# Kernel optimization log

Measured on AMD Instinct MI355X. Metric: run time of the kernel, lower is better.

The kernel has to match this reference:

```python
import jax, jax.numpy as jnp
import numpy as np

D = 128
N1, N2, N3, N4 = 100000, 200000, 300000, 400000


def setup_inputs() -> dict:
    key = jax.random.key(0)
    cnt = [0]

    def nrm(shape, scale=0.05):
        cnt[0] += 1
        return jax.random.normal(jax.random.fold_in(key, cnt[0]), shape, dtype=jnp.float32) * scale

    def rint(shape, hi):
        cnt[0] += 1
        return jax.random.randint(jax.random.fold_in(key, cnt[0]), shape, 0, hi)

    inp = {}
    inp["h"] = nrm((N1, D), 1.0)
    inp["idx2"] = rint((N2, 2), N1)
    inp["idx3"] = rint((N3, 3), N1)
    inp["idx4"] = rint((N4, 4), N1)
    # sequential_%L MLPs: Linear(L*D -> D) + relu, Linear(D->D)+relu, Linear(D->D)+relu
    for L in (1, 2, 3, 4):
        din = D * L
        inp["s%d_W0" % L] = nrm((din, D))
        inp["s%d_b0" % L] = nrm((D,))
        inp["s%d_W1" % L] = nrm((D, D))
        inp["s%d_b1" % L] = nrm((D,))
        inp["s%d_W2" % L] = nrm((D, D))
        inp["s%d_b2" % L] = nrm((D,))
    # per-feature output heads Linear(D -> 1)
    for f in ("sigma", "epsilon", "q"):
        inp["h1_%s_W" % f] = nrm((D, 1))
        inp["h1_%s_b" % f] = nrm((1,))
    for L in (2, 3, 4):
        for f in ("k", "eq"):
            inp["h%d_%s_W" % (L, f)] = nrm((D, 1))
            inp["h%d_%s_b" % (L, f)] = nrm((1,))
    return inp


def _mlp(x, W0, b0, W1, b1, W2, b2):
    x = jax.nn.relu(x @ W0 + b0)
    x = jax.nn.relu(x @ W1 + b1)
    return jax.nn.relu(x @ W2 + b2)


def _level(h, idx, p):
    # copy_u + mean with exactly one n1 neighbor per relationship slot == gather
    g = jnp.take(h, idx, axis=0)              # [N, K, D]
    N, K, Dd = g.shape
    xf = g.reshape(N, K * Dd)                 # concat h0..h_{K-1}
    xb = g[:, ::-1, :].reshape(N, K * Dd)     # concat reversed
    return _mlp(xf, *p) + _mlp(xb, *p)        # pool = torch.add


def reference(h, idx2, idx3, idx4,
              s1_W0, s1_b0, s1_W1, s1_b1, s1_W2, s1_b2,
              s2_W0, s2_b0, s2_W1, s2_b1, s2_W2, s2_b2,
              s3_W0, s3_b0, s3_W1, s3_b1, s3_W2, s3_b2,
              s4_W0, s4_b0, s4_W1, s4_b1, s4_W2, s4_b2,
              h1_sigma_W, h1_sigma_b, h1_epsilon_W, h1_epsilon_b, h1_q_W, h1_q_b,
              h2_k_W, h2_k_b, h2_eq_W, h2_eq_b,
              h3_k_W, h3_k_b, h3_eq_W, h3_eq_b,
              h4_k_W, h4_k_b, h4_eq_W, h4_eq_b):
    y1 = _mlp(h, s1_W0, s1_b0, s1_W1, s1_b1, s1_W2, s1_b2)
    sigma = y1 @ h1_sigma_W + h1_sigma_b
    epsilon = y1 @ h1_epsilon_W + h1_epsilon_b
    q = y1 @ h1_q_W + h1_q_b
    y2 = _level(h, idx2, (s2_W0, s2_b0, s2_W1, s2_b1, s2_W2, s2_b2))
    k2 = y2 @ h2_k_W + h2_k_b
    eq2 = y2 @ h2_eq_W + h2_eq_b
    y3 = _level(h, idx3, (s3_W0, s3_b0, s3_W1, s3_b1, s3_W2, s3_b2))
    k3 = y3 @ h3_k_W + h3_k_b
    eq3 = y3 @ h3_eq_W + h3_eq_b
    y4 = _level(h, idx4, (s4_W0, s4_b0, s4_W1, s4_b1, s4_W2, s4_b2))
    k4 = y4 @ h4_k_W + h4_k_b
    eq4 = y4 @ h4_eq_W + h4_eq_b
    return (sigma, epsilon, q, k2, eq2, k3, eq3, k4, eq4)
```

## Files before the change

### kernel.cpp

```cpp
#include <hip/hip_runtime.h>

typedef __attribute__((ext_vector_type(8))) _Float16 half8;
typedef __attribute__((ext_vector_type(4))) float f32x4;

#define N1_ 100000
#define N2_ 200000
#define N3_ 300000
#define N4_ 400000

typedef __attribute__((address_space(1))) const void gconst_t;
typedef __attribute__((address_space(3))) void lds_t;

__device__ __forceinline__ unsigned short f2h_bits(float x) {
  union { _Float16 h; unsigned short u; } cv;
  cv.h = (_Float16)x;
  return cv.u;
}

__device__ __forceinline__ f32x4 mfma16(half8 a, half8 b, f32x4 c) {
  return __builtin_amdgcn_mfma_f32_16x16x32_f16(a, b, c, 0, 0, 0);
}

__global__ void cvt_h_kernel(const float* __restrict__ h,
                             unsigned short* __restrict__ hf, int n4) {
  int i = blockIdx.x * blockDim.x + threadIdx.x;
  if (i >= n4) return;
  float4 v = reinterpret_cast<const float4*>(h)[i];
  ushort4 o;
  o.x = f2h_bits(v.x); o.y = f2h_bits(v.y);
  o.z = f2h_bits(v.z); o.w = f2h_bits(v.w);
  reinterpret_cast<ushort4*>(hf)[i] = o;
}

struct PackInfo {
  const float* W[12];
  int kt_base[13];
  int out_off[12];
};

__global__ void pack_w_kernel(PackInfo info, unsigned short* __restrict__ pw) {
  int b = blockIdx.x;
  int lane = threadIdx.x;
  int m = 0;
  while (m < 11 && b >= info.kt_base[m + 1]) ++m;
  int kt = b - info.kt_base[m];
  const float* W = info.W[m];
  int lr = lane & 15, kb = lane >> 4;
  unsigned short* outp = pw + info.out_off[m] + (size_t)kt * 4096 + lane * 8;
  #pragma unroll
  for (int nt = 0; nt < 8; ++nt) {
    #pragma unroll
    for (int j = 0; j < 8; ++j) {
      int krow = kt * 32 + kb * 8 + j;
      int col = nt * 16 + lr;
      outp[nt * 512 + j] = f2h_bits(W[(size_t)krow * 128 + col]);
    }
  }
}

template <int K, int NHEAD>
__global__ __launch_bounds__(256, 2) void level_kernel(
    const unsigned short* __restrict__ hf,
    const int* __restrict__ idx,
    const unsigned short* __restrict__ pw,
    const float* __restrict__ b0, const float* __restrict__ b1,
    const float* __restrict__ b2,
    const float* __restrict__ hw0, const float* __restrict__ hb0,
    float* __restrict__ out0,
    const float* __restrict__ hw1, const float* __restrict__ hb1,
    float* __restrict__ out1,
    const float* __restrict__ hw2, const float* __restrict__ hb2,
    float* __restrict__ out2,
    int N) {
  constexpr int NDIR = (K > 1) ? 2 : 1;
  constexpr int KT0 = 4 * K;
  constexpr int NPAIR = (K / 2) * 4;
  constexpr bool MID = (K % 2) != 0;

  __shared__ __align__(16) unsigned short bstage[2][4096];
  __shared__ __align__(16) unsigned short act[4][NDIR][2][2048];

  const int lane = threadIdx.x & 63;
  const int wid = threadIdx.x >> 6;
  const int lrow = lane & 15;
  const int kb = lane >> 4;

  const int wtile = (blockIdx.x * 4 + wid) * 2;
  const int maxtile = N / 16 - 1;
  int tile[2];
  bool wr[2];
  #pragma unroll
  for (int t = 0; t < 2; ++t) {
    wr[t] = (wtile + t <= maxtile);
    tile[t] = wr[t] ? (wtile + t) : maxtile;
  }

  int src[2][K];
  #pragma unroll
  for (int t = 0; t < 2; ++t)
    #pragma unroll
    for (int s = 0; s < K; ++s)
      src[t][s] = (K == 1) ? (tile[t] * 16 + lrow)
                           : idx[(size_t)(tile[t] * 16 + lrow) * K + s];

  auto stage = [&](int buf, const unsigned short* slab) {
    const unsigned short* g = slab + (wid * 2) * 512 + lane * 8;
    unsigned short* l = &bstage[buf][(wid * 2) * 512];
    __builtin_amdgcn_global_load_lds((gconst_t*)g, (lds_t*)l, 16, 0, 0);
    __builtin_amdgcn_global_load_lds((gconst_t*)(g + 512), (lds_t*)(l + 512), 16, 0, 0);
  };

  auto gfrag = [&](int segRow, int sub, half8* dst) {
    #pragma unroll
    for (int t = 0; t < 2; ++t)
      dst[t] = *reinterpret_cast<const half8*>(
          hf + (size_t)src[t][segRow] * 128 + sub * 32 + kb * 8);
  };

  f32x4 acc[2][NDIR][8];
  auto zero_acc = [&]() {
    #pragma unroll
    for (int t = 0; t < 2; ++t)
      #pragma unroll
      for (int d = 0; d < NDIR; ++d)
        #pragma unroll
        for (int nt = 0; nt < 8; ++nt) acc[t][d][nt] = f32x4{0.f, 0.f, 0.f, 0.f};
  };

  auto mfma_phase = [&](int buf, half8* af, half8* ab) {
    #pragma unroll
    for (int nt = 0; nt < 8; ++nt) {
      half8 bq = *reinterpret_cast<const half8*>(&bstage[buf][nt * 512 + lane * 8]);
      #pragma unroll
      for (int t = 0; t < 2; ++t) {
        acc[t][0][nt] = mfma16(af[t], bq, acc[t][0][nt]);
        if constexpr (NDIR == 2) acc[t][1][nt] = mfma16(ab[t], bq, acc[t][1][nt]);
      }
    }
  };

  auto actA = [&](int t, int d, int kt) -> half8 {
    unsigned off = (unsigned)(lrow * 256 + (kt * 32 + kb * 8) * 2) ^
                   ((unsigned)(lrow & 7) << 4);
    return *reinterpret_cast<const half8*>(
        reinterpret_cast<const unsigned char*>(&act[wid][d][t][0]) + off);
  };

  auto store_act = [&](int t, int d, const float* bias) {
    unsigned char* base = reinterpret_cast<unsigned char*>(&act[wid][d][t][0]);
    #pragma unroll
    for (int nt = 0; nt < 8; ++nt) {
      float bv = bias[nt * 16 + lrow];
      #pragma unroll
      for (int r = 0; r < 4; ++r) {
        float v = fmaxf(acc[t][d][nt][r] + bv, 0.f);
        int trow = 4 * kb + r;
        unsigned off = (unsigned)(trow * 256 + (nt * 16 + lrow) * 2) ^
                       ((unsigned)(trow & 7) << 4);
        *reinterpret_cast<unsigned short*>(base + off) = f2h_bits(v);
      }
    }
  };

  int cur = 0;
  zero_acc();

  half8 gA[2], gB[2], nA[2], nB[2];
  stage(cur, pw);
  gfrag(0, 0, gA);
  if constexpr (NPAIR > 0) gfrag(K - 1, 0, gB);
  __syncthreads();

  for (int pr = 0; pr < NPAIR; ++pr) {
    const int sp = pr >> 2, sub = pr & 3;
    const int slabB = (K - 1 - sp) * 4 + sub;
    stage(cur ^ 1, pw + (size_t)slabB * 4096);
    mfma_phase(cur, gA, gB);
    __syncthreads();
    cur ^= 1;
    if (pr + 1 < NPAIR) {
      const int sp2 = (pr + 1) >> 2, sub2 = (pr + 1) & 3;
      stage(cur ^ 1, pw + (size_t)(sp2 * 4 + sub2) * 4096);
      gfrag(sp2, sub2, nA);
      gfrag(K - 1 - sp2, sub2, nB);
    } else if constexpr (MID) {
      stage(cur ^ 1, pw + (size_t)(((K - 1) / 2) * 4) * 4096);
      gfrag((K - 1) / 2, 0, nA);
    } else {
      stage(cur ^ 1, pw + (size_t)KT0 * 4096);
    }
    mfma_phase(cur, gB, gA);
    __syncthreads();
    cur ^= 1;
    #pragma unroll
    for (int t = 0; t < 2; ++t) { gA[t] = nA[t]; gB[t] = nB[t]; }
  }

  if constexpr (MID) {
    const int mseg = (K - 1) / 2;
    for (int sub = 0; sub < 4; ++sub) {
      if (sub + 1 < 4) {
        stage(cur ^ 1, pw + (size_t)(mseg * 4 + sub + 1) * 4096);
        gfrag(mseg, sub + 1, nA);
      } else {
        stage(cur ^ 1, pw + (size_t)KT0 * 4096);
      }
      mfma_phase(cur, gA, gA);
      __syncthreads();
      cur ^= 1;
      #pragma unroll
      for (int t = 0; t < 2; ++t) gA[t] = nA[t];
    }
  }

  #pragma unroll
  for (int t = 0; t < 2; ++t)
    #pragma unroll
    for (int d = 0; d < NDIR; ++d) store_act(t, d, b0);

  const unsigned short* w1 = pw + (size_t)KT0 * 4096;
  #pragma unroll 1
  for (int layer = 1; layer <= 2; ++layer) {
    const unsigned short* w = (layer == 1) ? w1 : w1 + 16384;
    zero_acc();
    for (int kt = 0; kt < 4; ++kt) {
      if (kt + 1 < 4) stage(cur ^ 1, w + (size_t)(kt + 1) * 4096);
      else if (layer == 1) stage(cur ^ 1, w1 + 16384);
      half8 a[2][NDIR];
      #pragma unroll
      for (int t = 0; t < 2; ++t)
        #pragma unroll
        for (int d = 0; d < NDIR; ++d) a[t][d] = actA(t, d, kt);
      #pragma unroll
      for (int nt = 0; nt < 8; ++nt) {
        half8 bq = *reinterpret_cast<const half8*>(&bstage[cur][nt * 512 + lane * 8]);
        #pragma unroll
        for (int t = 0; t < 2; ++t)
          #pragma unroll
          for (int d = 0; d < NDIR; ++d)
            acc[t][d][nt] = mfma16(a[t][d], bq, acc[t][d][nt]);
      }
      if (!(layer == 2 && kt == 3)) {
        __syncthreads();
        cur ^= 1;
      }
    }
    if (layer == 1) {
      #pragma unroll
      for (int t = 0; t < 2; ++t)
        #pragma unroll
        for (int d = 0; d < NDIR; ++d) store_act(t, d, b1);
    }
  }

  const float* hws[3] = {hw0, hw1, hw2};
  const float* hbs[3] = {hb0, hb1, hb2};
  float* outs[3] = {out0, out1, out2};

  #pragma unroll
  for (int t = 0; t < 2; ++t) {
    f32x4 y[8];
    #pragma unroll
    for (int nt = 0; nt < 8; ++nt) {
      float bv = b2[nt * 16 + lrow];
      #pragma unroll
      for (int r = 0; r < 4; ++r) {
        float v = fmaxf(acc[t][0][nt][r] + bv, 0.f);
        if constexpr (NDIR == 2) v += fmaxf(acc[t][1][nt][r] + bv, 0.f);
        y[nt][r] = v;
      }
    }
    #pragma unroll
    for (int hd = 0; hd < NHEAD; ++hd) {
      float p[4] = {0.f, 0.f, 0.f, 0.f};
      #pragma unroll
      for (int nt = 0; nt < 8; ++nt) {
        float w = hws[hd][nt * 16 + lrow];
        #pragma unroll
        for (int r = 0; r < 4; ++r) p[r] += y[nt][r] * w;
      }
      #pragma unroll
      for (int m = 1; m < 16; m <<= 1) {
        #pragma unroll
        for (int r = 0; r < 4; ++r) p[r] += __shfl_xor(p[r], m, 64);
      }
      if (wr[t] && lrow < 4) {
        float pv = (lrow == 0) ? p[0] : (lrow == 1) ? p[1] : (lrow == 2) ? p[2] : p[3];
        outs[hd][tile[t] * 16 + 4 * kb + lrow] = pv + hbs[hd][0];
      }
    }
  }
}

extern "C" void kernel_launch(void* const* d_in, const int* in_sizes, int n_in,
                              void* d_out, int out_size, void* d_ws, size_t ws_size,
                              hipStream_t stream) {
  (void)in_sizes; (void)n_in; (void)out_size;

  const float* h = (const float*)d_in[0];
  const int* idx2 = (const int*)d_in[1];
  const int* idx3 = (const int*)d_in[2];
  const int* idx4 = (const int*)d_in[3];

  const float* sW[4][3];
  const float* sb[4][3];
  for (int L = 0; L < 4; ++L)
    for (int j = 0; j < 3; ++j) {
      sW[L][j] = (const float*)d_in[4 + L * 6 + j * 2];
      sb[L][j] = (const float*)d_in[4 + L * 6 + j * 2 + 1];
    }
  const float* hW[9];
  const float* hB[9];
  for (int i = 0; i < 9; ++i) {
    hW[i] = (const float*)d_in[28 + i * 2];
    hB[i] = (const float*)d_in[28 + i * 2 + 1];
  }

  size_t need = ((size_t)N1_ * 128 + 294912) * 2;
  if (ws_size < need) return;
  unsigned short* hf = (unsigned short*)d_ws;
  unsigned short* pw = hf + (size_t)N1_ * 128;

  cvt_h_kernel<<<(N1_ * 128 / 4 + 255) / 256, 256, 0, stream>>>(h, hf, N1_ * 128 / 4);

  PackInfo pi;
  const int din[12] = {128, 128, 128, 256, 128, 128, 384, 128, 128, 512, 128, 128};
  int ktb = 0, ooff = 0;
  for (int m = 0; m < 12; ++m) {
    pi.W[m] = sW[m / 3][m % 3];
    pi.kt_base[m] = ktb;
    pi.out_off[m] = ooff;
    ktb += din[m] / 32;
    ooff += din[m] * 128;
  }
  pi.kt_base[12] = ktb;
  pack_w_kernel<<<ktb, 64, 0, stream>>>(pi, pw);

  float* out = (float*)d_out;
  float* o_sigma = out;
  float* o_eps = out + N1_;
  float* o_q = out + 2 * N1_;
  float* o_k2 = out + 3 * N1_;
  float* o_eq2 = o_k2 + N2_;
  float* o_k3 = o_eq2 + N2_;
  float* o_eq3 = o_k3 + N3_;
  float* o_k4 = o_eq3 + N3_;
  float* o_eq4 = o_k4 + N4_;

  level_kernel<1, 3><<<(N1_ / 16 + 7) / 8, 256, 0, stream>>>(
      hf, nullptr, pw + pi.out_off[0], sb[0][0], sb[0][1], sb[0][2],
      hW[0], hB[0], o_sigma, hW[1], hB[1], o_eps, hW[2], hB[2], o_q, N1_);
  level_kernel<2, 2><<<(N2_ / 16 + 7) / 8, 256, 0, stream>>>(
      hf, idx2, pw + pi.out_off[3], sb[1][0], sb[1][1], sb[1][2],
      hW[3], hB[3], o_k2, hW[4], hB[4], o_eq2, nullptr, nullptr, nullptr, N2_);
  level_kernel<3, 2><<<(N3_ / 16 + 7) / 8, 256, 0, stream>>>(
      hf, idx3, pw + pi.out_off[6], sb[2][0], sb[2][1], sb[2][2],
      hW[5], hB[5], o_k3, hW[6], hB[6], o_eq3, nullptr, nullptr, nullptr, N3_);
  level_kernel<4, 2><<<(N4_ / 16 + 7) / 8, 256, 0, stream>>>(
      hf, idx4, pw + pi.out_off[9], sb[3][0], sb[3][1], sb[3][2],
      hW[7], hB[7], o_k4, hW[8], hB[8], o_eq4, nullptr, nullptr, nullptr, N4_);
}
```

Baseline: 449.5 us.

## Use 8 waves per block with one row tile per wave

Each block now runs 512 threads (8 waves), and each wave handles a single 16-row tile instead of two. The block still covers 128 rows, and each staged weight slab is now loaded with one global_load_lds per lane. Per-wave accumulators and gathered fragments are halved, which cuts register pressure and allows launch bounds of 4 blocks per CU for more latency hiding on the gathers. In exchange, each weight B-fragment read from LDS now feeds fewer MFMAs, and block-wide barriers synchronise twice as many waves.

```diff
diff --git a/kernel.cpp b/kernel.cpp
--- a/kernel.cpp
+++ b/kernel.cpp
@@ -59,7 +59,7 @@
 }
 
 template <int K, int NHEAD>
-__global__ __launch_bounds__(256, 2) void level_kernel(
+__global__ __launch_bounds__(512, 4) void level_kernel(
     const unsigned short* __restrict__ hf,
     const int* __restrict__ idx,
     const unsigned short* __restrict__ pw,
@@ -78,82 +78,67 @@
   constexpr bool MID = (K % 2) != 0;
 
   __shared__ __align__(16) unsigned short bstage[2][4096];
-  __shared__ __align__(16) unsigned short act[4][NDIR][2][2048];
+  __shared__ __align__(16) unsigned short act[8][NDIR][2048];
 
   const int lane = threadIdx.x & 63;
   const int wid = threadIdx.x >> 6;
   const int lrow = lane & 15;
   const int kb = lane >> 4;
 
-  const int wtile = (blockIdx.x * 4 + wid) * 2;
+  int tile = blockIdx.x * 8 + wid;
   const int maxtile = N / 16 - 1;
-  int tile[2];
-  bool wr[2];
-  #pragma unroll
-  for (int t = 0; t < 2; ++t) {
-    wr[t] = (wtile + t <= maxtile);
-    tile[t] = wr[t] ? (wtile + t) : maxtile;
-  }
-
-  int src[2][K];
-  #pragma unroll
-  for (int t = 0; t < 2; ++t)
-    #pragma unroll
-    for (int s = 0; s < K; ++s)
-      src[t][s] = (K == 1) ? (tile[t] * 16 + lrow)
-                           : idx[(size_t)(tile[t] * 16 + lrow) * K + s];
+  const bool wr = (tile <= maxtile);
+  if (!wr) tile = maxtile;
+
+  int src[K];
+  #pragma unroll
+  for (int s = 0; s < K; ++s)
+    src[s] = (K == 1) ? (tile * 16 + lrow)
+                      : idx[(size_t)(tile * 16 + lrow) * K + s];
 
   auto stage = [&](int buf, const unsigned short* slab) {
-    const unsigned short* g = slab + (wid * 2) * 512 + lane * 8;
-    unsigned short* l = &bstage[buf][(wid * 2) * 512];
+    const unsigned short* g = slab + wid * 512 + lane * 8;
+    unsigned short* l = &bstage[buf][wid * 512];
     __builtin_amdgcn_global_load_lds((gconst_t*)g, (lds_t*)l, 16, 0, 0);
-    __builtin_amdgcn_global_load_lds((gconst_t*)(g + 512), (lds_t*)(l + 512), 16, 0, 0);
-  };
-
-  auto gfrag = [&](int segRow, int sub, half8* dst) {
-    #pragma unroll
-    for (int t = 0; t < 2; ++t)
-      dst[t] = *reinterpret_cast<const half8*>(
-          hf + (size_t)src[t][segRow] * 128 + sub * 32 + kb * 8);
-  };
-
-  f32x4 acc[2][NDIR][8];
+  };
+
+  auto gfrag = [&](int segRow, int sub, half8& dst) {
+    dst = *reinterpret_cast<const half8*>(
+        hf + (size_t)src[segRow] * 128 + sub * 32 + kb * 8);
+  };
+
+  f32x4 acc[NDIR][8];
   auto zero_acc = [&]() {
     #pragma unroll
-    for (int t = 0; t < 2; ++t)
-      #pragma unroll
-      for (int d = 0; d < NDIR; ++d)
-        #pragma unroll
-        for (int nt = 0; nt < 8; ++nt) acc[t][d][nt] = f32x4{0.f, 0.f, 0.f, 0.f};
-  };
-
-  auto mfma_phase = [&](int buf, half8* af, half8* ab) {
+    for (int d = 0; d < NDIR; ++d)
+      #pragma unroll
+      for (int nt = 0; nt < 8; ++nt) acc[d][nt] = f32x4{0.f, 0.f, 0.f, 0.f};
+  };
+
+  auto mfma_phase = [&](int buf, half8 af, half8 ab) {
     #pragma unroll
     for (int nt = 0; nt < 8; ++nt) {
       half8 bq = *reinterpret_cast<const half8*>(&bstage[buf][nt * 512 + lane * 8]);
-      #pragma unroll
-      for (int t = 0; t < 2; ++t) {
-        acc[t][0][nt] = mfma16(af[t], bq, acc[t][0][nt]);
-        if constexpr (NDIR == 2) acc[t][1][nt] = mfma16(ab[t], bq, acc[t][1][nt]);
-      }
-    }
-  };
-
-  auto actA = [&](int t, int d, int kt) -> half8 {
+      acc[0][nt] = mfma16(af, bq, acc[0][nt]);
+      if constexpr (NDIR == 2) acc[1][nt] = mfma16(ab, bq, acc[1][nt]);
+    }
+  };
+
+  auto actA = [&](int d, int kt) -> half8 {
     unsigned off = (unsigned)(lrow * 256 + (kt * 32 + kb * 8) * 2) ^
                    ((unsigned)(lrow & 7) << 4);
     return *reinterpret_cast<const half8*>(
-        reinterpret_cast<const unsigned char*>(&act[wid][d][t][0]) + off);
-  };
-
-  auto store_act = [&](int t, int d, const float* bias) {
-    unsigned char* base = reinterpret_cast<unsigned char*>(&act[wid][d][t][0]);
+        reinterpret_cast<const unsigned char*>(&act[wid][d][0]) + off);
+  };
+
+  auto store_act = [&](int d, const float* bias) {
+    unsigned char* base = reinterpret_cast<unsigned char*>(&act[wid][d][0]);
     #pragma unroll
     for (int nt = 0; nt < 8; ++nt) {
       float bv = bias[nt * 16 + lrow];
       #pragma unroll
       for (int r = 0; r < 4; ++r) {
-        float v = fmaxf(acc[t][d][nt][r] + bv, 0.f);
+        float v = fmaxf(acc[d][nt][r] + bv, 0.f);
         int trow = 4 * kb + r;
         unsigned off = (unsigned)(trow * 256 + (nt * 16 + lrow) * 2) ^
                        ((unsigned)(trow & 7) << 4);
@@ -165,7 +150,7 @@
   int cur = 0;
   zero_acc();
 
-  half8 gA[2], gB[2], nA[2], nB[2];
+  half8 gA, gB, nA, nB;
   stage(cur, pw);
   gfrag(0, 0, gA);
   if constexpr (NPAIR > 0) gfrag(K - 1, 0, gB);
@@ -192,8 +177,7 @@
     mfma_phase(cur, gB, gA);
     __syncthreads();
     cur ^= 1;
-    #pragma unroll
-    for (int t = 0; t < 2; ++t) { gA[t] = nA[t]; gB[t] = nB[t]; }
+    gA = nA; gB = nB;
   }
 
   if constexpr (MID) {
@@ -208,15 +192,12 @@
       mfma_phase(cur, gA, gA);
       __syncthreads();
       cur ^= 1;
-      #pragma unroll
-      for (int t = 0; t < 2; ++t) gA[t] = nA[t];
-    }
-  }
-
-  #pragma unroll
-  for (int t = 0; t < 2; ++t)
-    #pragma unroll
-    for (int d = 0; d < NDIR; ++d) store_act(t, d, b0);
+      gA = nA;
+    }
+  }
+
+  #pragma unroll
+  for (int d = 0; d < NDIR; ++d) store_act(d, b0);
 
   const unsigned short* w1 = pw + (size_t)KT0 * 4096;
   #pragma unroll 1
@@ -226,19 +207,14 @@
     for (int kt = 0; kt < 4; ++kt) {
       if (kt + 1 < 4) stage(cur ^ 1, w + (size_t)(kt + 1) * 4096);
       else if (layer == 1) stage(cur ^ 1, w1 + 16384);
-      half8 a[2][NDIR];
-      #pragma unroll
-      for (int t = 0; t < 2; ++t)
-        #pragma unroll
-        for (int d = 0; d < NDIR; ++d) a[t][d] = actA(t, d, kt);
+      half8 a[NDIR];
+      #pragma unroll
+      for (int d = 0; d < NDIR; ++d) a[d] = actA(d, kt);
       #pragma unroll
       for (int nt = 0; nt < 8; ++nt) {
         half8 bq = *reinterpret_cast<const half8*>(&bstage[cur][nt * 512 + lane * 8]);
         #pragma unroll
-        for (int t = 0; t < 2; ++t)
-          #pragma unroll
-          for (int d = 0; d < NDIR; ++d)
-            acc[t][d][nt] = mfma16(a[t][d], bq, acc[t][d][nt]);
+        for (int d = 0; d < NDIR; ++d) acc[d][nt] = mfma16(a[d], bq, acc[d][nt]);
       }
       if (!(layer == 2 && kt == 3)) {
         __syncthreads();
@@ -247,47 +223,42 @@
     }
     if (layer == 1) {
       #pragma unroll
-      for (int t = 0; t < 2; ++t)
-        #pragma unroll
-        for (int d = 0; d < NDIR; ++d) store_act(t, d, b1);
+      for (int d = 0; d < NDIR; ++d) store_act(d, b1);
+    }
+  }
+
+  f32x4 y[8];
+  #pragma unroll
+  for (int nt = 0; nt < 8; ++nt) {
+    float bv = b2[nt * 16 + lrow];
+    #pragma unroll
+    for (int r = 0; r < 4; ++r) {
+      float v = fmaxf(acc[0][nt][r] + bv, 0.f);
+      if constexpr (NDIR == 2) v += fmaxf(acc[1][nt][r] + bv, 0.f);
+      y[nt][r] = v;
     }
   }
 
   const float* hws[3] = {hw0, hw1, hw2};
   const float* hbs[3] = {hb0, hb1, hb2};
   float* outs[3] = {out0, out1, out2};
-
-  #pragma unroll
-  for (int t = 0; t < 2; ++t) {
-    f32x4 y[8];
+  #pragma unroll
+  for (int hd = 0; hd < NHEAD; ++hd) {
+    float p[4] = {0.f, 0.f, 0.f, 0.f};
     #pragma unroll
     for (int nt = 0; nt < 8; ++nt) {
-      float bv = b2[nt * 16 + lrow];
-      #pragma unroll
-      for (int r = 0; r < 4; ++r) {
-        float v = fmaxf(acc[t][0][nt][r] + bv, 0.f);
-        if constexpr (NDIR == 2) v += fmaxf(acc[t][1][nt][r] + bv, 0.f);
-        y[nt][r] = v;
-      }
-    }
-    #pragma unroll
-    for (int hd = 0; hd < NHEAD; ++hd) {
-      float p[4] = {0.f, 0.f, 0.f, 0.f};
-      #pragma unroll
-      for (int nt = 0; nt < 8; ++nt) {
-        float w = hws[hd][nt * 16 + lrow];
-        #pragma unroll
-        for (int r = 0; r < 4; ++r) p[r] += y[nt][r] * w;
-      }
-      #pragma unroll
-      for (int m = 1; m < 16; m <<= 1) {
-        #pragma unroll
-        for (int r = 0; r < 4; ++r) p[r] += __shfl_xor(p[r], m, 64);
-      }
-      if (wr[t] && lrow < 4) {
-        float pv = (lrow == 0) ? p[0] : (lrow == 1) ? p[1] : (lrow == 2) ? p[2] : p[3];
-        outs[hd][tile[t] * 16 + 4 * kb + lrow] = pv + hbs[hd][0];
-      }
+      float w = hws[hd][nt * 16 + lrow];
+      #pragma unroll
+      for (int r = 0; r < 4; ++r) p[r] += y[nt][r] * w;
+    }
+    #pragma unroll
+    for (int m = 1; m < 16; m <<= 1) {
+      #pragma unroll
+      for (int r = 0; r < 4; ++r) p[r] += __shfl_xor(p[r], m, 64);
+    }
+    if (wr && lrow < 4) {
+      float pv = (lrow == 0) ? p[0] : (lrow == 1) ? p[1] : (lrow == 2) ? p[2] : p[3];
+      outs[hd][tile * 16 + 4 * kb + lrow] = pv + hbs[hd][0];
     }
   }
 }
@@ -347,16 +318,16 @@
   float* o_k4 = o_eq3 + N3_;
   float* o_eq4 = o_k4 + N4_;
 
-  level_kernel<1, 3><<<(N1_ / 16 + 7) / 8, 256, 0, stream>>>(
+  level_kernel<1, 3><<<(N1_ / 16 + 7) / 8, 512, 0, stream>>>(
       hf, nullptr, pw + pi.out_off[0], sb[0][0], sb[0][1], sb[0][2],
       hW[0], hB[0], o_sigma, hW[1], hB[1], o_eps, hW[2], hB[2], o_q, N1_);
-  level_kernel<2, 2><<<(N2_ / 16 + 7) / 8, 256, 0, stream>>>(
+  level_kernel<2, 2><<<(N2_ / 16 + 7) / 8, 512, 0, stream>>>(
       hf, idx2, pw + pi.out_off[3], sb[1][0], sb[1][1], sb[1][2],
       hW[3], hB[3], o_k2, hW[4], hB[4], o_eq2, nullptr, nullptr, nullptr, N2_);
-  level_kernel<3, 2><<<(N3_ / 16 + 7) / 8, 256, 0, stream>>>(
+  level_kernel<3, 2><<<(N3_ / 16 + 7) / 8, 512, 0, stream>>>(
       hf, idx3, pw + pi.out_off[6], sb[2][0], sb[2][1], sb[2][2],
       hW[5], hB[5], o_k3, hW[6], hB[6], o_eq3, nullptr, nullptr, nullptr, N3_);
-  level_kernel<4, 2><<<(N4_ / 16 + 7) / 8, 256, 0, stream>>>(
+  level_kernel<4, 2><<<(N4_ / 16 + 7) / 8, 512, 0, stream>>>(
       hf, idx4, pw + pi.out_off[9], sb[3][0], sb[3][1], sb[3][2],
       hW[7], hB[7], o_k4, hW[8], hB[8], o_eq4, nullptr, nullptr, nullptr, N4_);
 }
```

Result: slower. 590.0 us (+31.3%).
